# Performance work log

Measured on AMD Instinct MI355X. Metric: run time of the kernel, lower is better.

The kernel has to match this reference:

```python
import jax, jax.numpy as jnp
import numpy as np

NUM_NODES = 50000
NUM_EDGES = 800000
NUM_REL = 8
DIM = 64
NUM_BLOCKS = 8


def setup_inputs() -> dict:
    key = jax.random.key(0)
    ks = jax.random.split(key, 6)
    x = jax.random.normal(ks[0], (NUM_NODES, DIM), dtype=jnp.float32)
    source = jax.random.randint(ks[1], (NUM_EDGES,), 0, NUM_NODES)
    target = jax.random.randint(ks[2], (NUM_EDGES,), 0, NUM_NODES)
    edge_type = jax.random.randint(ks[3], (NUM_EDGES,), 0, NUM_REL)
    edge_weights = jax.random.uniform(ks[4], (NUM_EDGES,), dtype=jnp.float32)
    bs = DIM // NUM_BLOCKS
    # xavier_normal_ for (bs, bs) blocks: std = sqrt(2 / (fan_in + fan_out))
    std = (2.0 / (bs + bs)) ** 0.5
    blocks = std * jax.random.normal(ks[5], (NUM_REL, NUM_BLOCKS, bs, bs), dtype=jnp.float32)
    return {
        "x": x,
        "blocks": blocks,
        "edge_weights": edge_weights,
        "source": source,
        "target": target,
        "edge_type": edge_type,
    }


def reference(x, blocks, edge_weights, source, target, edge_type):
    # input_dim == output_dim -> use_horizontal_stacking is False -> vertically stacked path.
    # Vertically stacked adjacency: adj[(edge_type * N + target), source] = edge_weights,
    # so (adj @ x) is a per-(relation,target) scatter-add of weighted source features.
    n = x.shape[0]
    r, b, ib, ob = blocks.shape
    seg = edge_type * n + target                               # (E,) row index in stacked adj
    msgs = x[source] * edge_weights[:, None]                   # (E, in_dim)
    agg = jax.ops.segment_sum(msgs, seg, num_segments=r * n)   # (R*N, in_dim)
    agg = agg.reshape(r, n, b, ib)                             # (R, N, B, ib)
    out = jnp.einsum("rbio,rnbi->nbo", blocks, agg)            # sum over relations + block matmul
    return out.reshape(n, b * ob)                              # (N, out_dim)
```

## Files before the change

### kernel.cpp

```cpp
#include <hip/hip_runtime.h>


#define DIM 64
#define NBLK 8
#define BS 8
#define NREL 8
#define COL_PAD 12
#define LDS_T_TOTAL (NREL * NBLK * BS * COL_PAD)
#define CHUNK 64

#define TILE 4096
#define MAXB 1024
#define SORTW_CAP 4096

typedef unsigned int uint32;
typedef unsigned long long uint64;
typedef unsigned short uint16;

__global__ __launch_bounds__(512) void histA(
    const int* __restrict__ tgt, uint32* __restrict__ tile_hist,
    int num_edges, int nb)
{
    __shared__ uint32 h[MAXB];
    for (int i = threadIdx.x; i < nb; i += 512) h[i] = 0u;
    __syncthreads();
    const int base = blockIdx.x * TILE;
    const int end  = min(base + TILE, num_edges);
    for (int j = base + (int)threadIdx.x; j < end; j += 512)
        atomicAdd(&h[tgt[j] >> 6], 1u);
    __syncthreads();
    uint32* dst = tile_hist + (size_t)blockIdx.x * nb;
    for (int i = threadIdx.x; i < nb; i += 512) dst[i] = h[i];
}

__global__ __launch_bounds__(64) void colscan(
    uint32* __restrict__ tile_hist, uint32* __restrict__ totals,
    int nt, int nb)
{
    const int b    = blockIdx.x;
    const int lane = threadIdx.x;
    uint32 carry = 0;
    for (int t0 = 0; t0 < nt; t0 += 64) {
        const int t = t0 + lane;
        uint32 v = (t < nt) ? tile_hist[(size_t)t * nb + b] : 0u;
        uint32 xin = v;
#pragma unroll
        for (int d = 1; d < 64; d <<= 1) {
            uint32 tm = __shfl_up(xin, d, 64);
            if (lane >= d) xin += tm;
        }
        if (t < nt) tile_hist[(size_t)t * nb + b] = carry + xin - v;
        carry += __shfl(xin, 63, 64);
    }
    if (lane == 0) totals[b] = carry;
}

__global__ __launch_bounds__(512) void scan_totals(
    const uint32* __restrict__ totals, uint32* __restrict__ bbase, int nb)
{
    __shared__ uint32 wtot[8];
    const int tid = threadIdx.x, lane = tid & 63, wid = tid >> 6;
    uint32 carry = 0;
    const int nch = (nb + 511) >> 9;
    for (int c = 0; c < nch; ++c) {
        const int idx = (c << 9) + tid;
        uint32 v = (idx < nb) ? totals[idx] : 0u;
        uint32 xin = v;
#pragma unroll
        for (int d = 1; d < 64; d <<= 1) {
            uint32 t = __shfl_up(xin, d, 64);
            if (lane >= d) xin += t;
        }
        if (lane == 63) wtot[wid] = xin;
        __syncthreads();
        if (wid == 0) {
            uint32 y = (lane < 8) ? wtot[lane] : 0u;
#pragma unroll
            for (int d = 1; d < 8; d <<= 1) {
                uint32 t = __shfl_up(y, d, 64);
                if (lane >= d) y += t;
            }
            if (lane < 8) wtot[lane] = y;
        }
        __syncthreads();
        const uint32 base = carry + ((wid > 0) ? wtot[wid - 1] : 0u);
        if (idx < nb) bbase[idx] = base + xin - v;
        carry += wtot[7];
        __syncthreads();
    }
    if (tid == 0) bbase[nb] = carry;
}

__global__ __launch_bounds__(512) void scatterB(
    const int* __restrict__ src, const int* __restrict__ tgt,
    const int* __restrict__ etype, const float* __restrict__ ew,
    const uint32* __restrict__ tile_hist, const uint32* __restrict__ bbase,
    uint64* __restrict__ payload, int num_edges, int nb)
{
    __shared__ uint32 cur[MAXB];
    const uint32* th = tile_hist + (size_t)blockIdx.x * nb;
    for (int i = threadIdx.x; i < nb; i += 512) cur[i] = bbase[i] + th[i];
    __syncthreads();
    const int base = blockIdx.x * TILE;
    const int end  = min(base + TILE, num_edges);
    for (int j = base + (int)threadIdx.x; j < end; j += 512) {
        const int t = tgt[j];
        const uint32 pos = atomicAdd(&cur[t >> 6], 1u);
        const uint32 lo = (uint32)src[j] | ((uint32)etype[j] << 16)
                        | ((uint32)(t & 63) << 19);
        payload[pos] = ((uint64)__float_as_uint(ew[j]) << 32) | lo;
    }
}

__global__ __launch_bounds__(512) void sortW(
    uint64* __restrict__ payload, uint16* __restrict__ keyt,
    const uint32* __restrict__ bbase)
{
    __shared__ uint64 pay[SORTW_CAP];
    __shared__ uint32 hist[512];
    __shared__ uint32 cur[512];
    __shared__ uint32 wtot[8];
    const int tid = threadIdx.x;
    const int b   = blockIdx.x;
    const int beg = (int)bbase[b];
    const int cnt = (int)bbase[b + 1] - beg;

    if (cnt > SORTW_CAP) {
        for (int k = tid; k < cnt; k += 512) {
            const uint32 lo = (uint32)payload[beg + k];
            keyt[beg + k] = (uint16)((b << 6) | ((lo >> 19) & 63u));
        }
        return;
    }

    for (int k = tid; k < cnt; k += 512) pay[k] = payload[beg + k];
    hist[tid] = 0u;
    __syncthreads();
    for (int k = tid; k < cnt; k += 512)
        atomicAdd(&hist[((uint32)pay[k] >> 16) & 511u], 1u);
    __syncthreads();
    {
        const int lane = tid & 63, wid = tid >> 6;
        uint32 v = hist[tid], xin = v;
#pragma unroll
        for (int d = 1; d < 64; d <<= 1) {
            uint32 t = __shfl_up(xin, d, 64);
            if (lane >= d) xin += t;
        }
        if (lane == 63) wtot[wid] = xin;
        __syncthreads();
        if (wid == 0) {
            uint32 y = (lane < 8) ? wtot[lane] : 0u;
#pragma unroll
            for (int d = 1; d < 8; d <<= 1) {
                uint32 t = __shfl_up(y, d, 64);
                if (lane >= d) y += t;
            }
            if (lane < 8) wtot[lane] = y;
        }
        __syncthreads();
        cur[tid] = ((wid > 0) ? wtot[wid - 1] : 0u) + xin - v;
    }
    __syncthreads();
    for (int k = tid; k < cnt; k += 512) {
        const uint64 p   = pay[k];
        const uint32 key = ((uint32)p >> 16) & 511u;
        const uint32 pos = atomicAdd(&cur[key], 1u);
        payload[beg + pos] = p;
        keyt[beg + pos] = (uint16)((b << 6) | (key >> 3));
    }
}

#define XFORM(r_)                                                           \
    {                                                                       \
        const float* bp = bcol + (int)(r_) * (NBLK * BS * COL_PAD);         \
        const float4 c0 = *(const float4*)bp;                               \
        const float4 c1 = *(const float4*)(bp + 4);                         \
        const int bl = lane & ~7;                                           \
        oacc += c0.x * __shfl(agg, bl + 0, 64)                              \
              + c0.y * __shfl(agg, bl + 1, 64)                              \
              + c0.z * __shfl(agg, bl + 2, 64)                              \
              + c0.w * __shfl(agg, bl + 3, 64)                              \
              + c1.x * __shfl(agg, bl + 4, 64)                              \
              + c1.y * __shfl(agg, bl + 5, 64)                              \
              + c1.z * __shfl(agg, bl + 6, 64)                              \
              + c1.w * __shfl(agg, bl + 7, 64);                             \
        agg = 0.0f;                                                         \
    }

#define PREQ(i, lov, wv)                                                    \
    const uint32 lo##i = (lov);                                             \
    const float  w##i  = __uint_as_float(wv);                               \
    const float  xv##i = x[((size_t)(lo##i & 0xFFFFu) << 6) + lane];

#define ACC(i, t_)                                                          \
    {                                                                       \
        const int    tt = (int)(t_);                                        \
        const uint32 rr = (lo##i >> 16) & 7u;                               \
        if (tt != tcur || rr != rcur) {                                     \
            XFORM(rcur)                                                     \
            if (tt != tcur) {                                               \
                atomicAdd(out + (size_t)tcur * DIM + lane, oacc);           \
                oacc = 0.0f; tcur = tt;                                     \
            }                                                               \
            rcur = rr;                                                      \
        }                                                                   \
        agg = fmaf(w##i, xv##i, agg);                                       \
    }

__global__ __launch_bounds__(512) void rgcn_chunk_kernel(
    const float* __restrict__ x,
    const float* __restrict__ blocks,
    const uint64* __restrict__ payload,
    const uint16* __restrict__ keyt,
    float* __restrict__ out,
    int num_edges)
{
    __shared__ float blkT[LDS_T_TOTAL];
    for (int l = threadIdx.x; l < NREL * NBLK * BS * BS; l += blockDim.x) {
        const int o = l & 7;
        const int i = (l >> 3) & 7;
        const int rb = l >> 6;
        blkT[(rb * 8 + o) * COL_PAD + i] = blocks[l];
    }
    __syncthreads();

    const int lane = threadIdx.x & 63;
    const int wid  = __builtin_amdgcn_readfirstlane(threadIdx.x >> 6);
    const int wave = blockIdx.x * (int)(blockDim.x >> 6) + wid;
    const int beg  = wave * CHUNK;
    if (beg >= num_edges) return;
    const int end  = min(beg + CHUNK, num_edges);

    const int bq = lane >> 3;
    const int oo = lane & 7;
    const float* bcol = &blkT[(bq * 8 + oo) * COL_PAD];

    int    tcur = (int)keyt[beg];
    uint32 rcur = ((uint32)payload[beg] >> 16) & 7u;
    float  agg  = 0.0f;
    float  oacc = 0.0f;

    int j = beg;
    for (; j + 8 <= end; j += 8) {
        const uint4 q0 = *(const uint4*)(payload + j);
        const uint4 q1 = *(const uint4*)(payload + j + 2);
        const uint4 q2 = *(const uint4*)(payload + j + 4);
        const uint4 q3 = *(const uint4*)(payload + j + 6);
        const ushort4 ka = *(const ushort4*)(keyt + j);
        const ushort4 kb = *(const ushort4*)(keyt + j + 4);
        PREQ(0, q0.x, q0.y) PREQ(1, q0.z, q0.w)
        PREQ(2, q1.x, q1.y) PREQ(3, q1.z, q1.w)
        PREQ(4, q2.x, q2.y) PREQ(5, q2.z, q2.w)
        PREQ(6, q3.x, q3.y) PREQ(7, q3.z, q3.w)
        ACC(0, ka.x) ACC(1, ka.y) ACC(2, ka.z) ACC(3, ka.w)
        ACC(4, kb.x) ACC(5, kb.y) ACC(6, kb.z) ACC(7, kb.w)
    }
    for (; j < end; ++j) {
        const uint64 p0 = payload[j];
        const uint16 k0 = keyt[j];
        PREQ(0, (uint32)p0, (uint32)(p0 >> 32))
        ACC(0, k0)
    }
    XFORM(rcur)
    atomicAdd(out + (size_t)tcur * DIM + lane, oacc);
}

#define LDS_BLK_STRIDE 72
#define LDS_REL_STRIDE (NBLK * LDS_BLK_STRIDE)
#define LDS_TOTAL (NREL * LDS_REL_STRIDE)

__global__ __launch_bounds__(256) void rgcn_edge_kernel(
    const float* __restrict__ x, const float* __restrict__ blocks,
    const float* __restrict__ ew, const int* __restrict__ src,
    const int* __restrict__ tgt, const int* __restrict__ etype,
    float* __restrict__ out, int num_edges)
{
    __shared__ float blk[LDS_TOTAL];
    for (int l = threadIdx.x; l < NREL * NBLK * BS * BS; l += blockDim.x) {
        int r = l >> 9, bb = (l >> 6) & 7, rest = l & 63;
        blk[r * LDS_REL_STRIDE + bb * LDS_BLK_STRIDE + rest] = blocks[l];
    }
    __syncthreads();
    const int lane = threadIdx.x & 63;
    const int wave = blockIdx.x * (blockDim.x >> 6) + (threadIdx.x >> 6);
    const int total_waves = gridDim.x * (blockDim.x >> 6);
    const int b = lane >> 3;
    for (int e = wave; e < num_edges; e += total_waves) {
        const int s = src[e], t = tgt[e], r = etype[e];
        const float w = ew[e];
        const float4* xs = reinterpret_cast<const float4*>(x + (size_t)s * DIM + b * BS);
        const float4 v0 = xs[0], v1 = xs[1];
        const float* bb = &blk[r * LDS_REL_STRIDE + b * LDS_BLK_STRIDE + (lane & 7)];
        float a = v0.x * bb[0] + v0.y * bb[BS] + v0.z * bb[2 * BS] + v0.w * bb[3 * BS]
                + v1.x * bb[4 * BS] + v1.y * bb[5 * BS] + v1.z * bb[6 * BS] + v1.w * bb[7 * BS];
        atomicAdd(&out[(size_t)t * DIM + lane], w * a);
    }
}

extern "C" void kernel_launch(void* const* d_in, const int* in_sizes, int n_in,
                              void* d_out, int out_size, void* d_ws, size_t ws_size,
                              hipStream_t stream) {
    const float* x      = (const float*)d_in[0];
    const float* blocks = (const float*)d_in[1];
    const float* ew     = (const float*)d_in[2];
    const int*   src    = (const int*)d_in[3];
    const int*   tgt    = (const int*)d_in[4];
    const int*   etype  = (const int*)d_in[5];
    float* out = (float*)d_out;

    const int num_edges = in_sizes[2];
    const int num_nodes = in_sizes[0] / DIM;

    const int nb = (num_nodes + 63) >> 6;
    const int nt = (num_edges + TILE - 1) / TILE;

    const size_t payload_b = (size_t)num_edges * 8;
    const size_t keyt_b    = (size_t)num_edges * 2;
    const size_t th_b      = (size_t)nt * nb * 4;
    const size_t tot_b     = (size_t)nb * 4;
    const size_t bb_b      = (size_t)(nb + 1) * 4;
    const size_t need      = payload_b + keyt_b + th_b + tot_b + bb_b;

    if (nb > MAXB || ws_size < need) {
        hipMemsetAsync(d_out, 0, (size_t)out_size * sizeof(float), stream);
        rgcn_edge_kernel<<<2048, 256, 0, stream>>>(
            x, blocks, ew, src, tgt, etype, out, num_edges);
        return;
    }

    char* ws = (char*)d_ws;
    uint64* payload   = (uint64*)ws;
    uint16* keyt      = (uint16*)(ws + payload_b);
    uint32* tile_hist = (uint32*)(ws + payload_b + keyt_b);
    uint32* totals    = (uint32*)(ws + payload_b + keyt_b + th_b);
    uint32* bbase     = (uint32*)(ws + payload_b + keyt_b + th_b + tot_b);

    hipMemsetAsync(d_out, 0, (size_t)out_size * sizeof(float), stream);
    histA<<<nt, 512, 0, stream>>>(tgt, tile_hist, num_edges, nb);
    colscan<<<nb, 64, 0, stream>>>(tile_hist, totals, nt, nb);
    scan_totals<<<1, 512, 0, stream>>>(totals, bbase, nb);
    scatterB<<<nt, 512, 0, stream>>>(
        src, tgt, etype, ew, tile_hist, bbase, payload, num_edges, nb);
    sortW<<<nb, 512, 0, stream>>>(payload, keyt, bbase);

    const int waves   = (num_edges + CHUNK - 1) / CHUNK;
    const int gblocks = (waves + 7) / 8;
    rgcn_chunk_kernel<<<gblocks, 512, 0, stream>>>(
        x, blocks, payload, keyt, out, num_edges);
}
```

Baseline: 91.08 us.

## Replace per-tile histogram scan with global atomic bucket offsets; persistent chunk loop

The per-tile histogram matrix and its column scan are replaced by a global histogram built with atomics, a single scan, and atomic per-tile reservation of bucket ranges inside the scatter kernel. This removes one kernel launch and the strided column-scan pass. The aggregation kernel becomes grid-stride with a capped grid of 1024 blocks and chunk size 32, so each block's LDS weight table is loaded once and reused across many chunks. In exchange the scatter kernel recomputes the histogram, and placement order within a bucket becomes nondeterministic. That is harmless because sortW re-sorts each bucket.

```diff
diff --git a/kernel.cpp b/kernel.cpp
--- a/kernel.cpp
+++ b/kernel.cpp
@@ -7,7 +7,7 @@
 #define NREL 8
 #define COL_PAD 12
 #define LDS_T_TOTAL (NREL * NBLK * BS * COL_PAD)
-#define CHUNK 64
+#define CHUNK 32
 
 #define TILE 4096
 #define MAXB 1024
@@ -17,8 +17,8 @@
 typedef unsigned long long uint64;
 typedef unsigned short uint16;
 
-__global__ __launch_bounds__(512) void histA(
-    const int* __restrict__ tgt, uint32* __restrict__ tile_hist,
+__global__ __launch_bounds__(512) void histG(
+    const int* __restrict__ tgt, uint32* __restrict__ ghist,
     int num_edges, int nb)
 {
     __shared__ uint32 h[MAXB];
@@ -29,34 +29,13 @@
     for (int j = base + (int)threadIdx.x; j < end; j += 512)
         atomicAdd(&h[tgt[j] >> 6], 1u);
     __syncthreads();
-    uint32* dst = tile_hist + (size_t)blockIdx.x * nb;
-    for (int i = threadIdx.x; i < nb; i += 512) dst[i] = h[i];
-}
-
-__global__ __launch_bounds__(64) void colscan(
-    uint32* __restrict__ tile_hist, uint32* __restrict__ totals,
-    int nt, int nb)
-{
-    const int b    = blockIdx.x;
-    const int lane = threadIdx.x;
-    uint32 carry = 0;
-    for (int t0 = 0; t0 < nt; t0 += 64) {
-        const int t = t0 + lane;
-        uint32 v = (t < nt) ? tile_hist[(size_t)t * nb + b] : 0u;
-        uint32 xin = v;
-#pragma unroll
-        for (int d = 1; d < 64; d <<= 1) {
-            uint32 tm = __shfl_up(xin, d, 64);
-            if (lane >= d) xin += tm;
-        }
-        if (t < nt) tile_hist[(size_t)t * nb + b] = carry + xin - v;
-        carry += __shfl(xin, 63, 64);
-    }
-    if (lane == 0) totals[b] = carry;
-}
-
-__global__ __launch_bounds__(512) void scan_totals(
-    const uint32* __restrict__ totals, uint32* __restrict__ bbase, int nb)
+    for (int i = threadIdx.x; i < nb; i += 512)
+        if (h[i]) atomicAdd(&ghist[i], h[i]);
+}
+
+__global__ __launch_bounds__(512) void scan1(
+    const uint32* __restrict__ ghist, uint32* __restrict__ bbase,
+    uint32* __restrict__ gcur, int nb)
 {
     __shared__ uint32 wtot[8];
     const int tid = threadIdx.x, lane = tid & 63, wid = tid >> 6;
@@ -64,7 +43,7 @@
     const int nch = (nb + 511) >> 9;
     for (int c = 0; c < nch; ++c) {
         const int idx = (c << 9) + tid;
-        uint32 v = (idx < nb) ? totals[idx] : 0u;
+        uint32 v = (idx < nb) ? ghist[idx] : 0u;
         uint32 xin = v;
 #pragma unroll
         for (int d = 1; d < 64; d <<= 1) {
@@ -84,25 +63,35 @@
         }
         __syncthreads();
         const uint32 base = carry + ((wid > 0) ? wtot[wid - 1] : 0u);
-        if (idx < nb) bbase[idx] = base + xin - v;
+        if (idx < nb) {
+            const uint32 e = base + xin - v;
+            bbase[idx] = e;
+            gcur[idx]  = e;
+        }
         carry += wtot[7];
         __syncthreads();
     }
     if (tid == 0) bbase[nb] = carry;
 }
 
-__global__ __launch_bounds__(512) void scatterB(
+__global__ __launch_bounds__(512) void scatterG(
     const int* __restrict__ src, const int* __restrict__ tgt,
     const int* __restrict__ etype, const float* __restrict__ ew,
-    const uint32* __restrict__ tile_hist, const uint32* __restrict__ bbase,
-    uint64* __restrict__ payload, int num_edges, int nb)
-{
+    uint32* __restrict__ gcur, uint64* __restrict__ payload,
+    int num_edges, int nb)
+{
+    __shared__ uint32 h[MAXB];
     __shared__ uint32 cur[MAXB];
-    const uint32* th = tile_hist + (size_t)blockIdx.x * nb;
-    for (int i = threadIdx.x; i < nb; i += 512) cur[i] = bbase[i] + th[i];
+    for (int i = threadIdx.x; i < nb; i += 512) h[i] = 0u;
     __syncthreads();
     const int base = blockIdx.x * TILE;
     const int end  = min(base + TILE, num_edges);
+    for (int j = base + (int)threadIdx.x; j < end; j += 512)
+        atomicAdd(&h[tgt[j] >> 6], 1u);
+    __syncthreads();
+    for (int i = threadIdx.x; i < nb; i += 512)
+        if (h[i]) cur[i] = atomicAdd(&gcur[i], h[i]);
+    __syncthreads();
     for (int j = base + (int)threadIdx.x; j < end; j += 512) {
         const int t = tgt[j];
         const uint32 pos = atomicAdd(&cur[t >> 6], 1u);
@@ -227,43 +216,47 @@
 
     const int lane = threadIdx.x & 63;
     const int wid  = __builtin_amdgcn_readfirstlane(threadIdx.x >> 6);
-    const int wave = blockIdx.x * (int)(blockDim.x >> 6) + wid;
-    const int beg  = wave * CHUNK;
-    if (beg >= num_edges) return;
-    const int end  = min(beg + CHUNK, num_edges);
+    const int wave = blockIdx.x * 8 + wid;
+    const int W    = gridDim.x * 8;
 
     const int bq = lane >> 3;
     const int oo = lane & 7;
     const float* bcol = &blkT[(bq * 8 + oo) * COL_PAD];
 
-    int    tcur = (int)keyt[beg];
-    uint32 rcur = ((uint32)payload[beg] >> 16) & 7u;
-    float  agg  = 0.0f;
-    float  oacc = 0.0f;
-
-    int j = beg;
-    for (; j + 8 <= end; j += 8) {
-        const uint4 q0 = *(const uint4*)(payload + j);
-        const uint4 q1 = *(const uint4*)(payload + j + 2);
-        const uint4 q2 = *(const uint4*)(payload + j + 4);
-        const uint4 q3 = *(const uint4*)(payload + j + 6);
-        const ushort4 ka = *(const ushort4*)(keyt + j);
-        const ushort4 kb = *(const ushort4*)(keyt + j + 4);
-        PREQ(0, q0.x, q0.y) PREQ(1, q0.z, q0.w)
-        PREQ(2, q1.x, q1.y) PREQ(3, q1.z, q1.w)
-        PREQ(4, q2.x, q2.y) PREQ(5, q2.z, q2.w)
-        PREQ(6, q3.x, q3.y) PREQ(7, q3.z, q3.w)
-        ACC(0, ka.x) ACC(1, ka.y) ACC(2, ka.z) ACC(3, ka.w)
-        ACC(4, kb.x) ACC(5, kb.y) ACC(6, kb.z) ACC(7, kb.w)
-    }
-    for (; j < end; ++j) {
-        const uint64 p0 = payload[j];
-        const uint16 k0 = keyt[j];
-        PREQ(0, (uint32)p0, (uint32)(p0 >> 32))
-        ACC(0, k0)
-    }
-    XFORM(rcur)
-    atomicAdd(out + (size_t)tcur * DIM + lane, oacc);
+    const int nch = (num_edges + CHUNK - 1) / CHUNK;
+    for (int c = wave; c < nch; c += W) {
+        const int beg = c * CHUNK;
+        const int end = min(beg + CHUNK, num_edges);
+
+        int    tcur = (int)keyt[beg];
+        uint32 rcur = ((uint32)payload[beg] >> 16) & 7u;
+        float  agg  = 0.0f;
+        float  oacc = 0.0f;
+
+        int j = beg;
+        for (; j + 8 <= end; j += 8) {
+            const uint4 q0 = *(const uint4*)(payload + j);
+            const uint4 q1 = *(const uint4*)(payload + j + 2);
+            const uint4 q2 = *(const uint4*)(payload + j + 4);
+            const uint4 q3 = *(const uint4*)(payload + j + 6);
+            const ushort4 ka = *(const ushort4*)(keyt + j);
+            const ushort4 kb = *(const ushort4*)(keyt + j + 4);
+            PREQ(0, q0.x, q0.y) PREQ(1, q0.z, q0.w)
+            PREQ(2, q1.x, q1.y) PREQ(3, q1.z, q1.w)
+            PREQ(4, q2.x, q2.y) PREQ(5, q2.z, q2.w)
+            PREQ(6, q3.x, q3.y) PREQ(7, q3.z, q3.w)
+            ACC(0, ka.x) ACC(1, ka.y) ACC(2, ka.z) ACC(3, ka.w)
+            ACC(4, kb.x) ACC(5, kb.y) ACC(6, kb.z) ACC(7, kb.w)
+        }
+        for (; j < end; ++j) {
+            const uint64 p0 = payload[j];
+            const uint16 k0 = keyt[j];
+            PREQ(0, (uint32)p0, (uint32)(p0 >> 32))
+            ACC(0, k0)
+        }
+        XFORM(rcur)
+        atomicAdd(out + (size_t)tcur * DIM + lane, oacc);
+    }
 }
 
 #define LDS_BLK_STRIDE 72
@@ -317,10 +310,10 @@
 
     const size_t payload_b = (size_t)num_edges * 8;
     const size_t keyt_b    = (size_t)num_edges * 2;
-    const size_t th_b      = (size_t)nt * nb * 4;
-    const size_t tot_b     = (size_t)nb * 4;
+    const size_t gh_b      = (size_t)nb * 4;
     const size_t bb_b      = (size_t)(nb + 1) * 4;
-    const size_t need      = payload_b + keyt_b + th_b + tot_b + bb_b;
+    const size_t gc_b      = (size_t)nb * 4;
+    const size_t need      = payload_b + keyt_b + gh_b + bb_b + gc_b;
 
     if (nb > MAXB || ws_size < need) {
         hipMemsetAsync(d_out, 0, (size_t)out_size * sizeof(float), stream);
@@ -330,22 +323,22 @@
     }
 
     char* ws = (char*)d_ws;
-    uint64* payload   = (uint64*)ws;
-    uint16* keyt      = (uint16*)(ws + payload_b);
-    uint32* tile_hist = (uint32*)(ws + payload_b + keyt_b);
-    uint32* totals    = (uint32*)(ws + payload_b + keyt_b + th_b);
-    uint32* bbase     = (uint32*)(ws + payload_b + keyt_b + th_b + tot_b);
-
+    uint64* payload = (uint64*)ws;
+    uint16* keyt    = (uint16*)(ws + payload_b);
+    uint32* ghist   = (uint32*)(ws + payload_b + keyt_b);
+    uint32* bbase   = (uint32*)(ws + payload_b + keyt_b + gh_b);
+    uint32* gcur    = (uint32*)(ws + payload_b + keyt_b + gh_b + bb_b);
+
+    hipMemsetAsync(ghist, 0, gh_b, stream);
     hipMemsetAsync(d_out, 0, (size_t)out_size * sizeof(float), stream);
-    histA<<<nt, 512, 0, stream>>>(tgt, tile_hist, num_edges, nb);
-    colscan<<<nb, 64, 0, stream>>>(tile_hist, totals, nt, nb);
-    scan_totals<<<1, 512, 0, stream>>>(totals, bbase, nb);
-    scatterB<<<nt, 512, 0, stream>>>(
-        src, tgt, etype, ew, tile_hist, bbase, payload, num_edges, nb);
+    histG<<<nt, 512, 0, stream>>>(tgt, ghist, num_edges, nb);
+    scan1<<<1, 512, 0, stream>>>(ghist, bbase, gcur, nb);
+    scatterG<<<nt, 512, 0, stream>>>(
+        src, tgt, etype, ew, gcur, payload, num_edges, nb);
     sortW<<<nb, 512, 0, stream>>>(payload, keyt, bbase);
 
-    const int waves   = (num_edges + CHUNK - 1) / CHUNK;
-    const int gblocks = (waves + 7) / 8;
+    const int nchunks = (num_edges + CHUNK - 1) / CHUNK;
+    const int gblocks = min((nchunks + 7) / 8, 1024);
     rgcn_chunk_kernel<<<gblocks, 512, 0, stream>>>(
         x, blocks, payload, keyt, out, num_edges);
 }
```

After: 97.69 us. +7.3%, slower.
